# Kernel optimization log

Measured on AMD Instinct MI355X. Metric: run time of the kernel, lower is better.

Reference implementation:

```python
import jax, jax.numpy as jnp
import numpy as np

# Module config (matches init_kwargs)
N, D1, D2, BW, K = 8, 1024, 1024, 4, 4
D = D1 * D2
B = 4096
TEMPERATURE = 1.0


def setup_inputs() -> dict:
    key = jax.random.key(0)
    ks = jax.random.split(key, 6)
    x = jax.random.normal(ks[0], (B, N, D1), dtype=jnp.float32)
    # learned parameters (kaiming-ish normal init; exact init does not matter for correctness baseline)
    U = jax.random.normal(ks[1], (N, D, K), dtype=jnp.float32)
    V = jax.random.normal(ks[2], (BW, D, K), dtype=jnp.float32)
    scale = jax.random.normal(ks[3], (N, 1), dtype=jnp.float32)
    biasq = jax.random.normal(ks[4], (N, 1), dtype=jnp.float32)
    bias = jax.random.normal(ks[5], (N, D2), dtype=jnp.float32)
    return {"x": x, "U": U, "V": V, "scale": scale, "biasq": biasq, "bias": bias}


def reference(x, U, V, scale, biasq, bias):
    # twopow = [2^0, ..., 2^{bw-1}] (non-learned buffer)
    twopow = 2.0 ** jnp.arange(BW, dtype=jnp.float32)
    # CP contraction: Theta[n, b, d] = sum_k U[n,d,k] * V[b,d,k]
    Theta = jnp.einsum('ndk,bdk->nbd', U, V)  # (N, BW, D)
    # sigmoid with temperature T, input clamped to [-10, 10]
    soft_binary = jax.nn.sigmoid(jnp.clip(TEMPERATURE * Theta, -10.0, 10.0))
    # bit-weighted sum -> soft integer per weight element
    integer = jnp.einsum('nbd,b->nd', soft_binary, twopow)  # (N, D)
    # dequantize: scale * (integer - biasq - 2^bw)
    w = scale * (integer - biasq - 2.0 ** BW)  # (N, D)
    w = w.reshape(N, D1, D2)
    # batched per-ensemble-member GEMM: act[b,n,l] = sum_d x[b,n,d] * w[n,d,l]
    act = jnp.einsum('bnd,ndl->bnl', x, w) + bias  # bias broadcasts (N, D2)
    return act
```

## Files before the change

### kernel.cpp

```cpp
#include <hip/hip_runtime.h>


typedef __attribute__((ext_vector_type(8))) short short8;
typedef __attribute__((ext_vector_type(4))) float f32x4;
typedef __attribute__((ext_vector_type(4))) unsigned short ushort4v;

__device__ __forceinline__ unsigned short f2bf(float f) {
  union { float f; unsigned u; } a; a.f = f;
  unsigned u = a.u;
  u += 0x7fffu + ((u >> 16) & 1u);
  return (unsigned short)(u >> 16);
}

__global__ __launch_bounds__(256) void xcast_kernel(
    const float4* __restrict__ X4, ushort4v* __restrict__ Xb4) {
  const size_t idx = (size_t)blockIdx.x * 256 + threadIdx.x;
  const float4 v = X4[idx];
  const size_t flat = idx << 2;
  const int d1 = (int)(flat & 1023);
  const size_t nb = flat >> 10;
  const int nn = (int)(nb & 7);
  const size_t b = nb >> 3;
  ushort4v o;
  o.x = f2bf(v.x); o.y = f2bf(v.y); o.z = f2bf(v.z); o.w = f2bf(v.w);
  Xb4[(((size_t)nn << 22) + (b << 10) + (size_t)d1) >> 2] = o;
}

__global__ __launch_bounds__(256) void wgen_kernel(
    const float4* __restrict__ U4, const float4* __restrict__ V4,
    const float* __restrict__ scale, const float* __restrict__ biasq,
    unsigned short* __restrict__ Wt) {
  __shared__ float tiles[8][32][33];
  const int t = threadIdx.x;
  const int d1_0 = blockIdx.x * 32;
  const int d2_0 = blockIdx.y * 32;
#pragma unroll
  for (int i = 0; i < 4; i++) {
    const int e = t + 256 * i;
    const int r = e >> 5, c = e & 31;
    const size_t d = (size_t)(d1_0 + r) * 1024 + (size_t)(d2_0 + c);
    float4 u[8];
#pragma unroll
    for (int nn = 0; nn < 8; nn++) u[nn] = U4[((size_t)nn << 20) + d];
    float integ[8];
#pragma unroll
    for (int nn = 0; nn < 8; nn++) integ[nn] = 0.f;
#pragma unroll
    for (int b = 0; b < 4; b++) {
      const float4 v = V4[((size_t)b << 20) + d];
      const float pw = (float)(1 << b);
#pragma unroll
      for (int nn = 0; nn < 8; nn++) {
        float th = u[nn].x * v.x + u[nn].y * v.y + u[nn].z * v.z + u[nn].w * v.w;
        th = fminf(10.f, fmaxf(-10.f, th));
        integ[nn] += pw / (1.f + __expf(-th));
      }
    }
#pragma unroll
    for (int nn = 0; nn < 8; nn++) tiles[nn][r][c] = integ[nn];
  }
  __syncthreads();
#pragma unroll
  for (int i = 0; i < 4; i++) {
    const int e = t + 256 * i;
    const int orow = e >> 5, oc = e & 31;
#pragma unroll
    for (int nn = 0; nn < 8; nn++) {
      const float wval = scale[nn] * (tiles[nn][oc][orow] - biasq[nn] - 16.f);
      Wt[((size_t)nn << 20) + (size_t)(d2_0 + orow) * 1024 + (size_t)(d1_0 + oc)] =
          f2bf(wval);
    }
  }
}

#define AS1(p) ((const __attribute__((address_space(1))) void*)(p))
#define AS3(p) ((__attribute__((address_space(3))) void*)(p))

__global__ __launch_bounds__(256) void gemm_kernel(
    const unsigned short* __restrict__ Xb,
    const unsigned short* __restrict__ Wt,
    const float* __restrict__ bias,
    float* __restrict__ out) {
  __shared__ unsigned short As[128 * 32];
  __shared__ unsigned short Bs[128 * 32];
  const int t = threadIdx.x;
  const int wv = t >> 6;
  const int ln = t & 63;
  const int n = blockIdx.z;
  const int bm0 = blockIdx.x * 128;
  const int bn0 = blockIdx.y * 128;

  const unsigned short* Ag = Xb + ((size_t)n << 22);
  const unsigned short* Bg = Wt + ((size_t)n << 20);

  const int sr = wv * 16 + (ln >> 2);
  const int sk = (ln & 3) * 8;
  const unsigned short* a0 = Ag + (size_t)(bm0 + sr) * 1024 + sk;
  const unsigned short* a1 = a0 + 64 * 1024;
  const unsigned short* b0 = Bg + (size_t)(bn0 + sr) * 1024 + sk;
  const unsigned short* b1 = b0 + 64 * 1024;
  unsigned short* lA0 = As + wv * 512;
  unsigned short* lA1 = As + 2048 + wv * 512;
  unsigned short* lB0 = Bs + wv * 512;
  unsigned short* lB1 = Bs + 2048 + wv * 512;

  const int wm = wv >> 1, wn = wv & 1;
  const int lm = ln & 15;
  const int lk = (ln >> 4) * 8;
  const unsigned short* a_rd = As + (wm * 64 + lm) * 32 + lk;
  const unsigned short* b_rd = Bs + (wn * 64 + lm) * 32 + lk;

  f32x4 acc[4][4];
#pragma unroll
  for (int i = 0; i < 4; i++)
#pragma unroll
    for (int j = 0; j < 4; j++) acc[i][j] = (f32x4){0.f, 0.f, 0.f, 0.f};

  for (int k0 = 0; k0 < 1024; k0 += 32) {
    __builtin_amdgcn_global_load_lds(AS1(a0 + k0), AS3(lA0), 16, 0, 0);
    __builtin_amdgcn_global_load_lds(AS1(a1 + k0), AS3(lA1), 16, 0, 0);
    __builtin_amdgcn_global_load_lds(AS1(b0 + k0), AS3(lB0), 16, 0, 0);
    __builtin_amdgcn_global_load_lds(AS1(b1 + k0), AS3(lB1), 16, 0, 0);
    __syncthreads();
    short8 af[4], bfr[4];
#pragma unroll
    for (int i = 0; i < 4; i++) af[i] = *(const short8*)(a_rd + i * 512);
#pragma unroll
    for (int j = 0; j < 4; j++) bfr[j] = *(const short8*)(b_rd + j * 512);
#pragma unroll
    for (int i = 0; i < 4; i++)
#pragma unroll
      for (int j = 0; j < 4; j++)
        acc[i][j] =
            __builtin_amdgcn_mfma_f32_16x16x32_bf16(af[i], bfr[j], acc[i][j], 0, 0, 0);
    __syncthreads();
  }

  const int q = ln >> 4;
  const int row0 = bm0 + wm * 64 + q * 4;
  const int col0 = bn0 + wn * 64 + lm;
  float bv[4];
#pragma unroll
  for (int j = 0; j < 4; j++) bv[j] = bias[n * 1024 + col0 + j * 16];
#pragma unroll
  for (int i = 0; i < 4; i++) {
#pragma unroll
    for (int r = 0; r < 4; r++) {
      const int row = row0 + i * 16 + r;
      float* op = out + ((size_t)row * 8 + (size_t)n) * 1024;
#pragma unroll
      for (int j = 0; j < 4; j++) op[col0 + j * 16] = acc[i][j][r] + bv[j];
    }
  }
}

extern "C" void kernel_launch(void* const* d_in, const int* in_sizes, int n_in,
                              void* d_out, int out_size, void* d_ws, size_t ws_size,
                              hipStream_t stream) {
  const float* x     = (const float*)d_in[0];
  const float* U     = (const float*)d_in[1];
  const float* V     = (const float*)d_in[2];
  const float* scale = (const float*)d_in[3];
  const float* biasq = (const float*)d_in[4];
  const float* bias  = (const float*)d_in[5];
  float* out = (float*)d_out;

  unsigned short* Xb = (unsigned short*)d_ws;
  unsigned short* Wt = (unsigned short*)((char*)d_ws + (size_t)67108864);

  xcast_kernel<<<32768, 256, 0, stream>>>((const float4*)x, (ushort4v*)Xb);
  wgen_kernel<<<dim3(32, 32), 256, 0, stream>>>((const float4*)U, (const float4*)V,
                                                scale, biasq, Wt);
  gemm_kernel<<<dim3(32, 8, 8), 256, 0, stream>>>(Xb, Wt, bias, out);
}
```

Measured before the change: 474.1 us.

## Double GEMM K-tile to 64 with XOR-swizzled LDS layout

The GEMM main loop now stages a 64-wide K slice per iteration instead of 32, halving the number of barrier pairs and load rounds over the K dimension. The LDS tiles grow to 128x64 and the global-to-LDS column chunk index is XOR-swizzled with the row, and the fragment reads apply the same swizzle, to avoid bank conflicts on the wider rows. LDS use doubles per block, which may reduce occupancy, and there is still no double buffering.

```diff
diff --git a/kernel.cpp b/kernel.cpp
--- a/kernel.cpp
+++ b/kernel.cpp
@@ -81,8 +81,8 @@
     const unsigned short* __restrict__ Wt,
     const float* __restrict__ bias,
     float* __restrict__ out) {
-  __shared__ unsigned short As[128 * 32];
-  __shared__ unsigned short Bs[128 * 32];
+  __shared__ unsigned short As[128 * 64];
+  __shared__ unsigned short Bs[128 * 64];
   const int t = threadIdx.x;
   const int wv = t >> 6;
   const int ln = t & 63;
@@ -93,22 +93,19 @@
   const unsigned short* Ag = Xb + ((size_t)n << 22);
   const unsigned short* Bg = Wt + ((size_t)n << 20);
 
-  const int sr = wv * 16 + (ln >> 2);
-  const int sk = (ln & 3) * 8;
-  const unsigned short* a0 = Ag + (size_t)(bm0 + sr) * 1024 + sk;
-  const unsigned short* a1 = a0 + 64 * 1024;
-  const unsigned short* b0 = Bg + (size_t)(bn0 + sr) * 1024 + sk;
-  const unsigned short* b1 = b0 + 64 * 1024;
-  unsigned short* lA0 = As + wv * 512;
-  unsigned short* lA1 = As + 2048 + wv * 512;
-  unsigned short* lB0 = Bs + wv * 512;
-  unsigned short* lB1 = Bs + 2048 + wv * 512;
+  const int sr = wv * 8 + (ln >> 3);
+  const int sk = (((ln & 7) ^ (sr & 7)) * 8);
+  const unsigned short* ag = Ag + (size_t)(bm0 + sr) * 1024 + sk;
+  const unsigned short* bg = Bg + (size_t)(bn0 + sr) * 1024 + sk;
+  unsigned short* lA = As + wv * 512;
+  unsigned short* lB = Bs + wv * 512;
 
   const int wm = wv >> 1, wn = wv & 1;
   const int lm = ln & 15;
-  const int lk = (ln >> 4) * 8;
-  const unsigned short* a_rd = As + (wm * 64 + lm) * 32 + lk;
-  const unsigned short* b_rd = Bs + (wn * 64 + lm) * 32 + lk;
+  const int cq = ln >> 4;
+  const int sw = lm & 7;
+  const unsigned short* a_rd = As + (wm * 64 + lm) * 64;
+  const unsigned short* b_rd = Bs + (wn * 64 + lm) * 64;
 
   f32x4 acc[4][4];
 #pragma unroll
@@ -116,23 +113,30 @@
 #pragma unroll
     for (int j = 0; j < 4; j++) acc[i][j] = (f32x4){0.f, 0.f, 0.f, 0.f};
 
-  for (int k0 = 0; k0 < 1024; k0 += 32) {
-    __builtin_amdgcn_global_load_lds(AS1(a0 + k0), AS3(lA0), 16, 0, 0);
-    __builtin_amdgcn_global_load_lds(AS1(a1 + k0), AS3(lA1), 16, 0, 0);
-    __builtin_amdgcn_global_load_lds(AS1(b0 + k0), AS3(lB0), 16, 0, 0);
-    __builtin_amdgcn_global_load_lds(AS1(b1 + k0), AS3(lB1), 16, 0, 0);
+  for (int k0 = 0; k0 < 1024; k0 += 64) {
+#pragma unroll
+    for (int r = 0; r < 4; r++) {
+      __builtin_amdgcn_global_load_lds(AS1(ag + (size_t)(32 * r) * 1024 + k0),
+                                       AS3(lA + r * 2048), 16, 0, 0);
+      __builtin_amdgcn_global_load_lds(AS1(bg + (size_t)(32 * r) * 1024 + k0),
+                                       AS3(lB + r * 2048), 16, 0, 0);
+    }
     __syncthreads();
-    short8 af[4], bfr[4];
 #pragma unroll
-    for (int i = 0; i < 4; i++) af[i] = *(const short8*)(a_rd + i * 512);
+    for (int half = 0; half < 2; half++) {
+      const int off = ((half * 4 + cq) ^ sw) * 8;
+      short8 af[4], bfr[4];
 #pragma unroll
-    for (int j = 0; j < 4; j++) bfr[j] = *(const short8*)(b_rd + j * 512);
+      for (int i = 0; i < 4; i++) af[i] = *(const short8*)(a_rd + i * 1024 + off);
 #pragma unroll
-    for (int i = 0; i < 4; i++)
+      for (int j = 0; j < 4; j++) bfr[j] = *(const short8*)(b_rd + j * 1024 + off);
 #pragma unroll
-      for (int j = 0; j < 4; j++)
-        acc[i][j] =
-            __builtin_amdgcn_mfma_f32_16x16x32_bf16(af[i], bfr[j], acc[i][j], 0, 0, 0);
+      for (int i = 0; i < 4; i++)
+#pragma unroll
+        for (int j = 0; j < 4; j++)
+          acc[i][j] = __builtin_amdgcn_mfma_f32_16x16x32_bf16(af[i], bfr[j],
+                                                              acc[i][j], 0, 0, 0);
+    }
     __syncthreads();
   }
 
```

After: 469.1 us. No clear change (-1.1%).
